# Optimization experiments

Hardware: AMD Instinct MI355X
Metric: run time of the kernel (lower is better)

The kernel has to match this reference:

```python
import jax, jax.numpy as jnp
import numpy as np

V, D, T, B = 50257, 1024, 512, 4
H = 4 * D  # mlp hidden for encoder/decoder stand-ins


def setup_inputs() -> dict:
    key = jax.random.key(0)
    ks = jax.random.split(key, 16)
    sc = 0.02
    n = lambda k, shape: (jax.random.normal(k, shape, jnp.float32) * sc)
    return {
        'input_ids': jax.random.randint(ks[0], (B, 1, T), 0, V),
        'labels': jax.random.randint(ks[1], (B, T), 0, V),
        'wte': n(ks[2], (V, D)),
        'enc_w1': n(ks[3], (D, H)), 'enc_b1': jnp.zeros((H,), jnp.float32),
        'enc_w2': n(ks[4], (H, D)), 'enc_b2': jnp.zeros((D,), jnp.float32),
        'proj_w': n(ks[5], (D // 2, D)), 'proj_b': jnp.zeros((D,), jnp.float32),
        'dec_w1': n(ks[6], (D, H)), 'dec_b1': jnp.zeros((H,), jnp.float32),
        'dec_w2': n(ks[7], (H, D)), 'dec_b2': jnp.zeros((D,), jnp.float32),
        'lm_w': n(ks[8], (D, V)),
    }


def reference(input_ids, labels, wte, enc_w1, enc_b1, enc_w2, enc_b2,
              proj_w, proj_b, dec_w1, dec_b1, dec_w2, dec_b2, lm_w):
    dim = wte.shape[1]
    half = dim // 2
    tlen = input_ids.shape[-1]
    x = jnp.squeeze(input_ids, 1)                     # [B, T]
    h = wte[x]                                        # [B, T, D] embedding
    # encoder (token-wise MLP stand-in)
    h = jax.nn.gelu(h @ enc_w1 + enc_b1) @ enc_w2 + enc_b2
    e = h[:, -1, :]                                   # [B, D] last-token embedding
    # sliding overlapping windows: window i = e[i : i+dim//2] (single vectorized gather)
    idx = (jnp.arange(tlen)[:, None] + jnp.arange(half)[None, :]) % dim  # [T, D/2]
    windows = e[:, idx]                               # [B, T, D/2]
    p = windows @ proj_w + proj_b                     # [B, T, D]
    # decoder (token-wise MLP stand-in)
    d = jax.nn.gelu(p @ dec_w1 + dec_b1) @ dec_w2 + dec_b2
    logits = jnp.einsum('btd,dv->btv', d, lm_w)       # [B, T, V]
    output = jnp.transpose(logits, (0, 2, 1))         # [B, V, T] as in rearrange
    logp = jax.nn.log_softmax(output, axis=1)
    nll = -jnp.take_along_axis(logp, labels[:, None, :], axis=1)  # [B, 1, T]
    loss = jnp.mean(nll)
    return (loss, output)
```

## Files before the change

### kernel.cpp

```cpp
#include <hip/hip_runtime.h>

#define VSZ 50257
#define DSZ 1024
#define TSZ 512
#define BSZ 4
#define HSZ 4096
#define VPAD 50432
#define NCH (VPAD / 64)
#define NPOS 2048
#define QS 16.0f
#define DQS (1.0f / 256.0f)
#define CG 32
#define CPC 25

typedef __attribute__((ext_vector_type(4))) float f32x4;
typedef __attribute__((ext_vector_type(16))) float f32x16;
typedef __attribute__((ext_vector_type(4))) int i32x4;
typedef __attribute__((ext_vector_type(8))) int i32x8;

#define GLD16(gp, lp) __builtin_amdgcn_global_load_lds( \
  (const __attribute__((address_space(1))) unsigned int*)(gp), \
  (__attribute__((address_space(3))) unsigned int*)(lp), 16, 0, 0)

__device__ __forceinline__ float gelu_f(float x) {
  float x3 = x * x * x;
  float u = 0.7978845608028654f * (x + 0.044715f * x3);
  return 0.5f * x * (1.f + tanhf(u));
}

__device__ __forceinline__ unsigned char q8(float v) {
  return (unsigned char)__builtin_amdgcn_cvt_pk_fp8_f32(v * QS, v * QS, 0, 0);
}

__global__ __launch_bounds__(256) void transpose_all(
    const float* __restrict__ lm_w, const float* __restrict__ dw1,
    const float* __restrict__ dw2, const float* __restrict__ pw,
    unsigned char* __restrict__ lm8, unsigned char* __restrict__ w18,
    unsigned char* __restrict__ w28, unsigned char* __restrict__ p8) {
  __shared__ float tile[64][65];
  int bid = blockIdx.x;
  const float* src; unsigned char* dst; int R, C, Cpad, bx, by;
  if (bid < 12608)      { src = lm_w; dst = lm8; R = DSZ; C = VSZ; Cpad = VPAD; bx = bid % 788; by = bid / 788; }
  else if (bid < 13632) { int b = bid - 12608; src = dw1; dst = w18; R = DSZ; C = HSZ; Cpad = HSZ; bx = b % 64; by = b / 64; }
  else if (bid < 14656) { int b = bid - 13632; src = dw2; dst = w28; R = HSZ; C = DSZ; Cpad = DSZ; bx = b % 16; by = b / 16; }
  else                  { int b = bid - 14656; src = pw;  dst = p8;  R = 512; C = DSZ; Cpad = DSZ; bx = b % 16; by = b / 16; }
  int c0 = bx * 64, r0 = by * 64;
  int tid = threadIdx.x;
  int wv = tid >> 6, ln = tid & 63;
  int c = c0 + ln;
#pragma unroll 4
  for (int i = 0; i < 16; ++i) {
    int r = i * 4 + wv;
    tile[r][ln] = (c < C) ? src[(size_t)(r0 + r) * C + c] : 0.f;
  }
  __syncthreads();
  int ccb = tid >> 4;
  int r4 = (tid & 15) * 4;
#pragma unroll
  for (int j = 0; j < 4; ++j) {
    int cc = ccb + j * 16;
    if (c0 + cc >= Cpad) continue;
    unsigned int u = __builtin_amdgcn_cvt_pk_fp8_f32(QS * tile[r4 + 0][cc], QS * tile[r4 + 1][cc], 0, 0);
    u = __builtin_amdgcn_cvt_pk_fp8_f32(QS * tile[r4 + 2][cc], QS * tile[r4 + 3][cc], u, 1);
    *(unsigned int*)(dst + (size_t)(c0 + cc) * R + r0 + r4) = u;
  }
}

#define KS1 8
__global__ __launch_bounds__(256) void enc1p_kernel(const int* __restrict__ ids,
                                                    const float* __restrict__ wte,
                                                    const float* __restrict__ w1,
                                                    float* __restrict__ t1p) {
  __shared__ float ev[4][128];
  int h = blockIdx.x * 256 + threadIdx.x;
  int kc = blockIdx.y;
  for (int i = threadIdx.x; i < 512; i += 256) {
    int b = i >> 7, d = i & 127;
    int tok = ids[b * TSZ + (TSZ - 1)];
    ev[b][d] = wte[(size_t)tok * DSZ + kc * 128 + d];
  }
  __syncthreads();
  const float* w = w1 + (size_t)(kc * 128) * HSZ + h;
  float s0 = 0.f, s1 = 0.f, s2 = 0.f, s3 = 0.f;
#pragma unroll 4
  for (int d = 0; d < 128; ++d) {
    float wv = w[(size_t)d * HSZ];
    s0 += ev[0][d] * wv; s1 += ev[1][d] * wv;
    s2 += ev[2][d] * wv; s3 += ev[3][d] * wv;
  }
  t1p[((size_t)(0 * KS1 + kc)) * HSZ + h] = s0;
  t1p[((size_t)(1 * KS1 + kc)) * HSZ + h] = s1;
  t1p[((size_t)(2 * KS1 + kc)) * HSZ + h] = s2;
  t1p[((size_t)(3 * KS1 + kc)) * HSZ + h] = s3;
}

#define KS2 16
__global__ __launch_bounds__(256) void enc2p_kernel(const float* __restrict__ t1p,
                                                    const float* __restrict__ b1,
                                                    const float* __restrict__ w2,
                                                    float* __restrict__ ep) {
  __shared__ float ts[4][256];
  int i = blockIdx.x * 256 + threadIdx.x;
  int kc = blockIdx.y;
  int h = kc * 256 + threadIdx.x;
  float bv = b1[h];
#pragma unroll
  for (int b = 0; b < 4; ++b) {
    float s0 = bv;
#pragma unroll
    for (int cc = 0; cc < KS1; ++cc) s0 += t1p[((size_t)(b * KS1 + cc)) * HSZ + h];
    ts[b][threadIdx.x] = gelu_f(s0);
  }
  __syncthreads();
  const float* w = w2 + (size_t)(kc * 256) * DSZ + i;
  float a0 = 0.f, a1 = 0.f, a2 = 0.f, a3 = 0.f;
#pragma unroll 4
  for (int j = 0; j < 256; ++j) {
    float wv = w[(size_t)j * DSZ];
    a0 += ts[0][j] * wv; a1 += ts[1][j] * wv;
    a2 += ts[2][j] * wv; a3 += ts[3][j] * wv;
  }
  ep[((size_t)(0 * KS2 + kc)) * DSZ + i] = a0;
  ep[((size_t)(1 * KS2 + kc)) * DSZ + i] = a1;
  ep[((size_t)(2 * KS2 + kc)) * DSZ + i] = a2;
  ep[((size_t)(3 * KS2 + kc)) * DSZ + i] = a3;
}

__global__ __launch_bounds__(256) void enc2c_kernel(const float* __restrict__ ep,
                                                    const float* __restrict__ b2,
                                                    float* __restrict__ e) {
  int idx = blockIdx.x * 256 + threadIdx.x;
  int b = idx >> 10, i = idx & (DSZ - 1);
  float s = b2[i];
#pragma unroll
  for (int kc = 0; kc < KS2; ++kc) s += ep[((size_t)(b * KS2 + kc)) * DSZ + i];
  e[idx] = s;
}

__global__ void win8_kernel(const float* __restrict__ e, unsigned char* __restrict__ win8) {
  int blk = blockIdx.x;
  int b = blk >> 9, t = blk & 511;
  const float* eb = e + b * DSZ;
  for (int j = threadIdx.x; j < 512; j += 256)
    win8[(size_t)blk * 512 + j] = q8(eb[t + j]);
}

template<int GELU>
__global__ __launch_bounds__(256, 3) void gemm8(
    const unsigned char* __restrict__ A, const unsigned char* __restrict__ Bm,
    const float* __restrict__ bias, unsigned char* __restrict__ out8,
    int NT, int N, int K) {
  __shared__ __align__(16) char SM[49152];
  const int tid = threadIdx.x;
  const int lane = tid & 63;
  const int wave = tid >> 6;
  const int wr = (wave >> 1) * 64, wc = (wave & 1) * 64;
  const int l15 = lane & 15, l4 = lane >> 4;

  const int cpx = (int)gridDim.x >> 3;
  const int wg = ((int)blockIdx.x & 7) * cpx + ((int)blockIdx.x >> 3);
  const int m0 = (wg / NT) * 128, n0 = (wg % NT) * 128;

  f32x4 acc[4][4];
#pragma unroll
  for (int i = 0; i < 4; ++i)
#pragma unroll
    for (int j = 0; j < 4; ++j) acc[i][j] = (f32x4){0.f, 0.f, 0.f, 0.f};

  const int ppair = lane & 3;
  const int row0 = wave * 16 + (lane >> 2);
  const int row1 = row0 + 64;
  const int og0 = (ppair - (row0 >> 1)) & 3;
  const int og1 = (ppair - (row1 >> 1)) & 3;
  const unsigned char* a0 = A + (size_t)(m0 + row0) * K + og0 * 16;
  const unsigned char* a1 = A + (size_t)(m0 + row1) * K + og1 * 16;
  const unsigned char* b0 = Bm + (size_t)(n0 + row0) * K + og0 * 16;
  const unsigned char* b1 = Bm + (size_t)(n0 + row1) * K + og1 * 16;

#define STG8(tt, bufb) do { \
    GLD16(a0 + (size_t)(tt) * 64, SM + (bufb) + wave * 1024); \
    GLD16(a1 + (size_t)(tt) * 64, SM + (bufb) + 4096 + wave * 1024); \
    GLD16(b0 + (size_t)(tt) * 64, SM + (bufb) + 8192 + wave * 1024); \
    GLD16(b1 + (size_t)(tt) * 64, SM + (bufb) + 12288 + wave * 1024); \
  } while (0)

  const int KT = K >> 6;
  STG8(0, 0);
  if (KT > 1) STG8(1, 16384);
  int cb = 0;
  for (int t = 0; t < KT; ++t) {
    if (t + 2 < KT) {
      int nb = cb + 32768; if (nb >= 49152) nb -= 49152;
      STG8(t + 2, nb);
      asm volatile("s_waitcnt vmcnt(8)" ::: "memory");
    } else if (t + 1 < KT) {
      asm volatile("s_waitcnt vmcnt(4)" ::: "memory");
    } else {
      asm volatile("s_waitcnt vmcnt(0)" ::: "memory");
    }
    __builtin_amdgcn_s_barrier();
    asm volatile("" ::: "memory");
    long af[4][2], bfr[4][2];
#pragma unroll
    for (int mi = 0; mi < 4; ++mi) {
      const int row = wr + mi * 16 + l15;
#pragma unroll
      for (int kk = 0; kk < 2; ++kk) {
        const int ph = ((kk * 2 + (l4 >> 1)) + (row >> 1)) & 3;
        af[mi][kk] = *(const long*)(SM + cb + row * 64 + ph * 16 + (l4 & 1) * 8);
      }
    }
#pragma unroll
    for (int ni = 0; ni < 4; ++ni) {
      const int row = wc + ni * 16 + l15;
#pragma unroll
      for (int kk = 0; kk < 2; ++kk) {
        const int ph = ((kk * 2 + (l4 >> 1)) + (row >> 1)) & 3;
        bfr[ni][kk] = *(const long*)(SM + cb + 8192 + row * 64 + ph * 16 + (l4 & 1) * 8);
      }
    }
    asm volatile("s_waitcnt lgkmcnt(0)" ::: "memory");
    __builtin_amdgcn_sched_barrier(0);
    __builtin_amdgcn_s_setprio(1);
#pragma unroll
    for (int kk = 0; kk < 2; ++kk)
#pragma unroll
      for (int mi = 0; mi < 4; ++mi)
#pragma unroll
        for (int ni = 0; ni < 4; ++ni)
          acc[mi][ni] = __builtin_amdgcn_mfma_f32_16x16x32_fp8_fp8(
              af[mi][kk], bfr[ni][kk], acc[mi][ni], 0, 0, 0);
    __builtin_amdgcn_s_setprio(0);
    __builtin_amdgcn_s_barrier();
    asm volatile("" ::: "memory");
    cb += 16384; if (cb >= 49152) cb = 0;
  }
#undef STG8

#pragma unroll
  for (int ni = 0; ni < 4; ++ni) {
    int n = n0 + wc + ni * 16 + l15;
    float bv = bias[n];
#pragma unroll
    for (int mi = 0; mi < 4; ++mi) {
#pragma unroll
      for (int r = 0; r < 4; ++r) {
        int m = m0 + wr + mi * 16 + l4 * 4 + r;
        float v = acc[mi][ni][r] * DQS + bv;
        if (GELU) v = gelu_f(v);
        out8[(size_t)m * N + n] = q8(v);
      }
    }
  }
}

__global__ __launch_bounds__(256, 3) void gemmLM(
    const unsigned char* __restrict__ A, const unsigned char* __restrict__ Bm,
    float* __restrict__ outF, float* __restrict__ pm, float* __restrict__ ps) {
  __shared__ __align__(16) char SM[49152];
  const int tid = threadIdx.x;
  const int lane = tid & 63;
  const int wave = tid >> 6;
  const int wr = (wave >> 1) * 64, wc = (wave & 1) * 64;
  const int l31 = lane & 31, hi = lane >> 5;

  const int cpx = (int)gridDim.x >> 3;
  const int wg = ((int)blockIdx.x & 7) * cpx + ((int)blockIdx.x >> 3);
  const int m0 = (wg >> 4) * 128, n0 = (wg & 15) * 128;

  f32x16 acc[2][2];
#pragma unroll
  for (int i = 0; i < 2; ++i)
#pragma unroll
    for (int j = 0; j < 2; ++j)
#pragma unroll
      for (int r = 0; r < 16; ++r) acc[i][j][r] = 0.f;

  const int ppair = lane & 3;
  const int row0 = wave * 16 + (lane >> 2);
  const int row1 = row0 + 64;
  const int og0 = (ppair - (row0 >> 1)) & 3;
  const int og1 = (ppair - (row1 >> 1)) & 3;
  const unsigned char* a0 = A + (size_t)(m0 + row0) * DSZ + og0 * 16;
  const unsigned char* a1 = A + (size_t)(m0 + row1) * DSZ + og1 * 16;
  const unsigned char* b0 = Bm + (size_t)(n0 + row0) * DSZ + og0 * 16;
  const unsigned char* b1 = Bm + (size_t)(n0 + row1) * DSZ + og1 * 16;

#define STGL(tt, bufb) do { \
    GLD16(a0 + (size_t)(tt) * 64, SM + (bufb) + wave * 1024); \
    GLD16(a1 + (size_t)(tt) * 64, SM + (bufb) + 4096 + wave * 1024); \
    GLD16(b0 + (size_t)(tt) * 64, SM + (bufb) + 8192 + wave * 1024); \
    GLD16(b1 + (size_t)(tt) * 64, SM + (bufb) + 12288 + wave * 1024); \
  } while (0)

  STGL(0, 0);
  STGL(1, 16384);
  int cb = 0;
  for (int t = 0; t < 16; ++t) {
    if (t + 2 < 16) {
      int nb = cb + 32768; if (nb >= 49152) nb -= 49152;
      STGL(t + 2, nb);
      asm volatile("s_waitcnt vmcnt(8)" ::: "memory");
    } else if (t + 1 < 16) {
      asm volatile("s_waitcnt vmcnt(4)" ::: "memory");
    } else {
      asm volatile("s_waitcnt vmcnt(0)" ::: "memory");
    }
    __builtin_amdgcn_s_barrier();
    asm volatile("" ::: "memory");
    i32x8 a8[2], b8[2];
#pragma unroll
    for (int mf = 0; mf < 2; ++mf) {
      const int row = wr + mf * 32 + l31;
      const char* base = SM + cb + row * 64;
      const int ph0 = (2 * hi + (row >> 1)) & 3;
      const int ph1 = (2 * hi + 1 + (row >> 1)) & 3;
      i32x4 q01 = *(const i32x4*)(base + ph0 * 16);
      i32x4 q23 = *(const i32x4*)(base + ph1 * 16);
      a8[mf] = __builtin_shufflevector(q01, q23, 0, 1, 2, 3, 4, 5, 6, 7);
    }
#pragma unroll
    for (int nf = 0; nf < 2; ++nf) {
      const int row = wc + nf * 32 + l31;
      const char* base = SM + cb + 8192 + row * 64;
      const int ph0 = (2 * hi + (row >> 1)) & 3;
      const int ph1 = (2 * hi + 1 + (row >> 1)) & 3;
      i32x4 q01 = *(const i32x4*)(base + ph0 * 16);
      i32x4 q23 = *(const i32x4*)(base + ph1 * 16);
      b8[nf] = __builtin_shufflevector(q01, q23, 0, 1, 2, 3, 4, 5, 6, 7);
    }
    asm volatile("s_waitcnt lgkmcnt(0)" ::: "memory");
    __builtin_amdgcn_sched_barrier(0);
    __builtin_amdgcn_s_setprio(1);
#pragma unroll
    for (int mf = 0; mf < 2; ++mf)
#pragma unroll
      for (int nf = 0; nf < 2; ++nf)
        acc[mf][nf] = __builtin_amdgcn_mfma_scale_f32_32x32x64_f8f6f4(
            a8[mf], b8[nf], acc[mf][nf], 0, 0, 0, 123, 0, 123);
    __builtin_amdgcn_s_setprio(0);
    __builtin_amdgcn_s_barrier();
    asm volatile("" ::: "memory");
    cb += 16384; if (cb >= 49152) cb = 0;
  }
#undef STGL

  const int ch = (m0 + wr) >> 6;
#pragma unroll
  for (int nf = 0; nf < 2; ++nf) {
    const int pos = n0 + wc + nf * 32 + l31;
    float mloc = -1e30f, sloc = 0.f;
#pragma unroll
    for (int mf = 0; mf < 2; ++mf) {
      const int vb = m0 + wr + mf * 32 + 4 * hi;
#pragma unroll
      for (int r = 0; r < 16; ++r) {
        const int v = vb + (r & 3) + 8 * (r >> 2);
        if (v < VSZ) mloc = fmaxf(mloc, acc[mf][nf][r]);
      }
    }
#pragma unroll
    for (int mf = 0; mf < 2; ++mf) {
      const int vb = m0 + wr + mf * 32 + 4 * hi;
#pragma unroll
      for (int r = 0; r < 16; ++r) {
        const int v = vb + (r & 3) + 8 * (r >> 2);
        if (v < VSZ) sloc += __expf(acc[mf][nf][r] - mloc);
      }
    }
    {
      float mo = __shfl_xor(mloc, 32, 64);
      float so = __shfl_xor(sloc, 32, 64);
      float nm = fmaxf(mloc, mo);
      sloc = sloc * __expf(mloc - nm) + so * __expf(mo - nm);
      mloc = nm;
    }
    if (hi == 0) {
      pm[(size_t)ch * NPOS + pos] = mloc;
      ps[(size_t)ch * NPOS + pos] = sloc;
    }
  }

  float* epi = (float*)SM;
  const int bb = n0 >> 9, t0 = n0 & 511;
  float* outG = outF + 1 + (size_t)bb * VSZ * TSZ + t0;
  const int trow = tid >> 5;
  const int lofs = (tid & 31) * 4;
#pragma unroll
  for (int q = 0; q < 4; ++q) {
    __builtin_amdgcn_s_barrier();
    asm volatile("" ::: "memory");
    if ((wave >> 1) == (q >> 1)) {
      const int mf = q & 1;
#pragma unroll
      for (int nf = 0; nf < 2; ++nf)
#pragma unroll
        for (int r = 0; r < 16; ++r)
          epi[((r & 3) + 8 * (r >> 2) + 4 * hi) * 132 + wc + nf * 32 + l31] =
              acc[mf][nf][r];
    }
    __builtin_amdgcn_s_barrier();
    asm volatile("" ::: "memory");
#pragma unroll
    for (int p = 0; p < 4; ++p) {
      int row = p * 8 + trow;
      int v = m0 + q * 32 + row;
      if (v < VSZ) {
        f32x4 val = *(const f32x4*)&epi[row * 132 + lofs];
        float* gp = outG + (size_t)v * TSZ + lofs;
        __builtin_nontemporal_store(val[0], gp + 0);
        __builtin_nontemporal_store(val[1], gp + 1);
        __builtin_nontemporal_store(val[2], gp + 2);
        __builtin_nontemporal_store(val[3], gp + 3);
      }
    }
  }
}

__global__ __launch_bounds__(256) void lsestage1_kernel(const float* __restrict__ pm,
                                                        const float* __restrict__ ps,
                                                        float* __restrict__ pm2,
                                                        float* __restrict__ ps2) {
  int pos = (blockIdx.x & 7) * 256 + threadIdx.x;
  int cg = blockIdx.x >> 3;
  int c0 = cg * CPC;
  int c1 = c0 + CPC; if (c1 > NCH) c1 = NCH;
  float m = -1e30f, s = 0.f;
  for (int c = c0; c < c1; ++c) {
    float cm = pm[(size_t)c * NPOS + pos];
    float cs = ps[(size_t)c * NPOS + pos];
    float nm = fmaxf(m, cm);
    s = s * __expf(m - nm) + cs * __expf(cm - nm);
    m = nm;
  }
  pm2[(size_t)cg * NPOS + pos] = m;
  ps2[(size_t)cg * NPOS + pos] = s;
}

__global__ __launch_bounds__(256) void lsemerge_kernel(const float* __restrict__ pm2,
                                                       const float* __restrict__ ps2,
                                                       const float* __restrict__ outF,
                                                       const int* __restrict__ labels,
                                                       float* __restrict__ contrib) {
  int pos = blockIdx.x * 256 + threadIdx.x;
  float m[4] = {-1e30f, -1e30f, -1e30f, -1e30f};
  float s[4] = {0.f, 0.f, 0.f, 0.f};
  for (int c = 0; c < CG; c += 4) {
#pragma unroll
    for (int j = 0; j < 4; ++j) {
      float cm = pm2[(size_t)(c + j) * NPOS + pos];
      float cs = ps2[(size_t)(c + j) * NPOS + pos];
      float nm = fmaxf(m[j], cm);
      s[j] = s[j] * __expf(m[j] - nm) + cs * __expf(cm - nm);
      m[j] = nm;
    }
  }
#pragma unroll
  for (int j = 1; j < 4; ++j) {
    float nm = fmaxf(m[0], m[j]);
    s[0] = s[0] * __expf(m[0] - nm) + s[j] * __expf(m[j] - nm);
    m[0] = nm;
  }
  float lse = m[0] + logf(s[0]);
  int b = pos >> 9, t = pos & 511;
  int lab = labels[pos];
  float x = outF[1 + (size_t)b * VSZ * TSZ + (size_t)lab * TSZ + t];
  contrib[pos] = lse - x;
}

__global__ __launch_bounds__(256) void lossfinal_kernel(const float* __restrict__ contrib,
                                                        float* __restrict__ dout) {
  __shared__ float red[256];
  int tid = threadIdx.x;
  float a = 0.f;
  for (int i = tid; i < NPOS; i += 256) a += contrib[i];
  red[tid] = a;
  __syncthreads();
  for (int off = 128; off; off >>= 1) {
    if (tid < off) red[tid] += red[tid + off];
    __syncthreads();
  }
  if (tid == 0) dout[0] = red[0] / (float)NPOS;
}

extern "C" void kernel_launch(void* const* d_in, const int* in_sizes, int n_in,
                              void* d_out, int out_size, void* d_ws, size_t ws_size,
                              hipStream_t stream) {
  const int* input_ids = (const int*)d_in[0];
  const int* labels    = (const int*)d_in[1];
  const float* wte     = (const float*)d_in[2];
  const float* enc_w1  = (const float*)d_in[3];
  const float* enc_b1  = (const float*)d_in[4];
  const float* enc_w2  = (const float*)d_in[5];
  const float* enc_b2  = (const float*)d_in[6];
  const float* proj_w  = (const float*)d_in[7];
  const float* proj_b  = (const float*)d_in[8];
  const float* dec_w1  = (const float*)d_in[9];
  const float* dec_b1  = (const float*)d_in[10];
  const float* dec_w2  = (const float*)d_in[11];
  const float* dec_b2  = (const float*)d_in[12];
  const float* lm_w    = (const float*)d_in[13];
  float* outF = (float*)d_out;

  char* w = (char*)d_ws;
  size_t off = 0;
  unsigned char* lm8  = (unsigned char*)(w + off); off += (size_t)VPAD * DSZ;
  unsigned char* w18  = (unsigned char*)(w + off); off += (size_t)HSZ * DSZ;
  unsigned char* w28  = (unsigned char*)(w + off); off += (size_t)DSZ * HSZ;
  unsigned char* p8   = (unsigned char*)(w + off); off += (size_t)DSZ * 512;
  unsigned char* win8 = (unsigned char*)(w + off); off += (size_t)NPOS * 512;
  unsigned char* pbuf8= (unsigned char*)(w + off); off += (size_t)NPOS * DSZ;
  unsigned char* abuf8= (unsigned char*)(w + off); off += (size_t)NPOS * HSZ;
  unsigned char* dbuf8= (unsigned char*)(w + off); off += (size_t)NPOS * DSZ;
  float* e      = (float*)(w + off);  off += (size_t)BSZ * DSZ * 4;
  float* t1p    = (float*)(w + off);  off += (size_t)BSZ * KS1 * HSZ * 4;
  float* ep     = (float*)(w + off);  off += (size_t)BSZ * KS2 * DSZ * 4;
  float* contrib= (float*)(w + off);  off += (size_t)NPOS * 4;
  float* pm     = (float*)(w + off);  off += (size_t)NCH * NPOS * 4;
  float* ps     = (float*)(w + off);  off += (size_t)NCH * NPOS * 4;
  float* pm2    = (float*)(w + off);  off += (size_t)CG * NPOS * 4;
  float* ps2    = (float*)(w + off);  off += (size_t)CG * NPOS * 4;
  (void)ws_size; (void)in_sizes; (void)n_in; (void)out_size;

  transpose_all<<<14784, 256, 0, stream>>>(lm_w, dec_w1, dec_w2, proj_w, lm8, w18, w28, p8);

  enc1p_kernel<<<dim3(HSZ / 256, KS1), 256, 0, stream>>>(input_ids, wte, enc_w1, t1p);
  enc2p_kernel<<<dim3(DSZ / 256, KS2), 256, 0, stream>>>(t1p, enc_b1, enc_w2, ep);
  enc2c_kernel<<<dim3(BSZ * DSZ / 256), 256, 0, stream>>>(ep, enc_b2, e);
  win8_kernel<<<2048, 256, 0, stream>>>(e, win8);

  gemm8<0><<<128, 256, 0, stream>>>(win8, p8, proj_b, pbuf8, 8, DSZ, 512);
  gemm8<1><<<512, 256, 0, stream>>>(pbuf8, w18, dec_b1, abuf8, 32, HSZ, DSZ);
  gemm8<0><<<128, 256, 0, stream>>>(abuf8, w28, dec_b2, dbuf8, 8, DSZ, HSZ);
  gemmLM<<<6304, 256, 0, stream>>>(lm8, dbuf8, outF, pm, ps);

  lsestage1_kernel<<<256, 256, 0, stream>>>(pm, ps, pm2, ps2);
  lsemerge_kernel<<<dim3(NPOS / 256), 256, 0, stream>>>(pm2, ps2, outF, labels, contrib);
  lossfinal_kernel<<<1, 256, 0, stream>>>(contrib, outF);
}
```

Measured before the change: 395.3 us.

## Fuse encoder kernels into transpose and window kernels, drop LDS-staged LM epilogue

Folds the first encoder partial-GEMM into the weight transpose/quantize launch as extra blocks and folds the encoder reduction into the window quantization kernel, removing two kernel launches and the intermediate buffer. The LM-head GEMM epilogue now writes accumulators straight to global memory with nontemporal scalar stores instead of staging through LDS for coalesced vector stores. That removes barriers and LDS traffic, but the output writes become strided and less coalesced across the 400MB logits tensor.

```diff
diff --git a/kernel.cpp b/kernel.cpp
--- a/kernel.cpp
+++ b/kernel.cpp
@@ -32,20 +32,51 @@
   return (unsigned char)__builtin_amdgcn_cvt_pk_fp8_f32(v * QS, v * QS, 0, 0);
 }
 
+#define KS1 8
+#define KS2 16
 __global__ __launch_bounds__(256) void transpose_all(
     const float* __restrict__ lm_w, const float* __restrict__ dw1,
     const float* __restrict__ dw2, const float* __restrict__ pw,
     unsigned char* __restrict__ lm8, unsigned char* __restrict__ w18,
-    unsigned char* __restrict__ w28, unsigned char* __restrict__ p8) {
+    unsigned char* __restrict__ w28, unsigned char* __restrict__ p8,
+    const int* __restrict__ ids, const float* __restrict__ wte,
+    const float* __restrict__ w1, float* __restrict__ t1p) {
   __shared__ float tile[64][65];
   int bid = blockIdx.x;
+  int tid = threadIdx.x;
+
+  if (bid >= 14784) {
+    int eb = bid - 14784;
+    int h = (eb & 15) * 256 + tid;
+    int kc = eb >> 4;
+    float (*ev)[128] = (float(*)[128])tile;
+    for (int i = tid; i < 512; i += 256) {
+      int b = i >> 7, d = i & 127;
+      int tok = ids[b * TSZ + (TSZ - 1)];
+      ev[b][d] = wte[(size_t)tok * DSZ + kc * 128 + d];
+    }
+    __syncthreads();
+    const float* w = w1 + (size_t)(kc * 128) * HSZ + h;
+    float s0 = 0.f, s1 = 0.f, s2 = 0.f, s3 = 0.f;
+#pragma unroll 4
+    for (int d = 0; d < 128; ++d) {
+      float wv = w[(size_t)d * HSZ];
+      s0 += ev[0][d] * wv; s1 += ev[1][d] * wv;
+      s2 += ev[2][d] * wv; s3 += ev[3][d] * wv;
+    }
+    t1p[((size_t)(0 * KS1 + kc)) * HSZ + h] = s0;
+    t1p[((size_t)(1 * KS1 + kc)) * HSZ + h] = s1;
+    t1p[((size_t)(2 * KS1 + kc)) * HSZ + h] = s2;
+    t1p[((size_t)(3 * KS1 + kc)) * HSZ + h] = s3;
+    return;
+  }
+
   const float* src; unsigned char* dst; int R, C, Cpad, bx, by;
   if (bid < 12608)      { src = lm_w; dst = lm8; R = DSZ; C = VSZ; Cpad = VPAD; bx = bid % 788; by = bid / 788; }
   else if (bid < 13632) { int b = bid - 12608; src = dw1; dst = w18; R = DSZ; C = HSZ; Cpad = HSZ; bx = b % 64; by = b / 64; }
   else if (bid < 14656) { int b = bid - 13632; src = dw2; dst = w28; R = HSZ; C = DSZ; Cpad = DSZ; bx = b % 16; by = b / 16; }
   else                  { int b = bid - 14656; src = pw;  dst = p8;  R = 512; C = DSZ; Cpad = DSZ; bx = b % 16; by = b / 16; }
   int c0 = bx * 64, r0 = by * 64;
-  int tid = threadIdx.x;
   int wv = tid >> 6, ln = tid & 63;
   int c = c0 + ln;
 #pragma unroll 4
@@ -66,35 +97,6 @@
   }
 }
 
-#define KS1 8
-__global__ __launch_bounds__(256) void enc1p_kernel(const int* __restrict__ ids,
-                                                    const float* __restrict__ wte,
-                                                    const float* __restrict__ w1,
-                                                    float* __restrict__ t1p) {
-  __shared__ float ev[4][128];
-  int h = blockIdx.x * 256 + threadIdx.x;
-  int kc = blockIdx.y;
-  for (int i = threadIdx.x; i < 512; i += 256) {
-    int b = i >> 7, d = i & 127;
-    int tok = ids[b * TSZ + (TSZ - 1)];
-    ev[b][d] = wte[(size_t)tok * DSZ + kc * 128 + d];
-  }
-  __syncthreads();
-  const float* w = w1 + (size_t)(kc * 128) * HSZ + h;
-  float s0 = 0.f, s1 = 0.f, s2 = 0.f, s3 = 0.f;
-#pragma unroll 4
-  for (int d = 0; d < 128; ++d) {
-    float wv = w[(size_t)d * HSZ];
-    s0 += ev[0][d] * wv; s1 += ev[1][d] * wv;
-    s2 += ev[2][d] * wv; s3 += ev[3][d] * wv;
-  }
-  t1p[((size_t)(0 * KS1 + kc)) * HSZ + h] = s0;
-  t1p[((size_t)(1 * KS1 + kc)) * HSZ + h] = s1;
-  t1p[((size_t)(2 * KS1 + kc)) * HSZ + h] = s2;
-  t1p[((size_t)(3 * KS1 + kc)) * HSZ + h] = s3;
-}
-
-#define KS2 16
 __global__ __launch_bounds__(256) void enc2p_kernel(const float* __restrict__ t1p,
                                                     const float* __restrict__ b1,
                                                     const float* __restrict__ w2,
@@ -126,23 +128,19 @@
   ep[((size_t)(3 * KS2 + kc)) * DSZ + i] = a3;
 }
 
-__global__ __launch_bounds__(256) void enc2c_kernel(const float* __restrict__ ep,
-                                                    const float* __restrict__ b2,
-                                                    float* __restrict__ e) {
-  int idx = blockIdx.x * 256 + threadIdx.x;
-  int b = idx >> 10, i = idx & (DSZ - 1);
-  float s = b2[i];
-#pragma unroll
-  for (int kc = 0; kc < KS2; ++kc) s += ep[((size_t)(b * KS2 + kc)) * DSZ + i];
-  e[idx] = s;
-}
-
-__global__ void win8_kernel(const float* __restrict__ e, unsigned char* __restrict__ win8) {
+__global__ __launch_bounds__(256) void win8_kernel(const float* __restrict__ ep,
+                                                   const float* __restrict__ b2,
+                                                   unsigned char* __restrict__ win8) {
   int blk = blockIdx.x;
   int b = blk >> 9, t = blk & 511;
-  const float* eb = e + b * DSZ;
-  for (int j = threadIdx.x; j < 512; j += 256)
-    win8[(size_t)blk * 512 + j] = q8(eb[t + j]);
+  const float* epb = ep + (size_t)b * KS2 * DSZ;
+  for (int j = threadIdx.x; j < 512; j += 256) {
+    int d = t + j;
+    float s = b2[d];
+#pragma unroll
+    for (int kc = 0; kc < KS2; ++kc) s += epb[(size_t)kc * DSZ + d];
+    win8[(size_t)blk * 512 + j] = q8(s);
+  }
 }
 
 template<int GELU>
@@ -381,37 +379,18 @@
     }
   }
 
-  float* epi = (float*)SM;
   const int bb = n0 >> 9, t0 = n0 & 511;
   float* outG = outF + 1 + (size_t)bb * VSZ * TSZ + t0;
-  const int trow = tid >> 5;
-  const int lofs = (tid & 31) * 4;
-#pragma unroll
-  for (int q = 0; q < 4; ++q) {
-    __builtin_amdgcn_s_barrier();
-    asm volatile("" ::: "memory");
-    if ((wave >> 1) == (q >> 1)) {
-      const int mf = q & 1;
-#pragma unroll
-      for (int nf = 0; nf < 2; ++nf)
-#pragma unroll
-        for (int r = 0; r < 16; ++r)
-          epi[((r & 3) + 8 * (r >> 2) + 4 * hi) * 132 + wc + nf * 32 + l31] =
-              acc[mf][nf][r];
-    }
-    __builtin_amdgcn_s_barrier();
-    asm volatile("" ::: "memory");
-#pragma unroll
-    for (int p = 0; p < 4; ++p) {
-      int row = p * 8 + trow;
-      int v = m0 + q * 32 + row;
-      if (v < VSZ) {
-        f32x4 val = *(const f32x4*)&epi[row * 132 + lofs];
-        float* gp = outG + (size_t)v * TSZ + lofs;
-        __builtin_nontemporal_store(val[0], gp + 0);
-        __builtin_nontemporal_store(val[1], gp + 1);
-        __builtin_nontemporal_store(val[2], gp + 2);
-        __builtin_nontemporal_store(val[3], gp + 3);
+#pragma unroll
+  for (int mf = 0; mf < 2; ++mf) {
+#pragma unroll
+    for (int nf = 0; nf < 2; ++nf) {
+      const int pcol = wc + nf * 32 + l31;
+#pragma unroll
+      for (int r = 0; r < 16; ++r) {
+        const int vrow = m0 + wr + mf * 32 + (r & 3) + 8 * (r >> 2) + 4 * hi;
+        if (vrow < VSZ)
+          __builtin_nontemporal_store(acc[mf][nf][r], outG + (size_t)vrow * TSZ + pcol);
       }
     }
   }
@@ -512,7 +491,6 @@
   unsigned char* pbuf8= (unsigned char*)(w + off); off += (size_t)NPOS * DSZ;
   unsigned char* abuf8= (unsigned char*)(w + off); off += (size_t)NPOS * HSZ;
   unsigned char* dbuf8= (unsigned char*)(w + off); off += (size_t)NPOS * DSZ;
-  float* e      = (float*)(w + off);  off += (size_t)BSZ * DSZ * 4;
   float* t1p    = (float*)(w + off);  off += (size_t)BSZ * KS1 * HSZ * 4;
   float* ep     = (float*)(w + off);  off += (size_t)BSZ * KS2 * DSZ * 4;
   float* contrib= (float*)(w + off);  off += (size_t)NPOS * 4;
@@ -522,12 +500,12 @@
   float* ps2    = (float*)(w + off);  off += (size_t)CG * NPOS * 4;
   (void)ws_size; (void)in_sizes; (void)n_in; (void)out_size;
 
-  transpose_all<<<14784, 256, 0, stream>>>(lm_w, dec_w1, dec_w2, proj_w, lm8, w18, w28, p8);
-
-  enc1p_kernel<<<dim3(HSZ / 256, KS1), 256, 0, stream>>>(input_ids, wte, enc_w1, t1p);
+  transpose_all<<<14912, 256, 0, stream>>>(lm_w, dec_w1, dec_w2, proj_w,
+                                           lm8, w18, w28, p8,
+                                           input_ids, wte, enc_w1, t1p);
+
   enc2p_kernel<<<dim3(DSZ / 256, KS2), 256, 0, stream>>>(t1p, enc_b1, enc_w2, ep);
-  enc2c_kernel<<<dim3(BSZ * DSZ / 256), 256, 0, stream>>>(ep, enc_b2, e);
-  win8_kernel<<<2048, 256, 0, stream>>>(e, win8);
+  win8_kernel<<<2048, 256, 0, stream>>>(ep, enc_b2, win8);
 
   gemm8<0><<<128, 256, 0, stream>>>(win8, p8, proj_b, pbuf8, 8, DSZ, 512);
   gemm8<1><<<512, 256, 0, stream>>>(pbuf8, w18, dec_b1, abuf8, 32, HSZ, DSZ);
```

After: 522.7 us. 32.2% more time.
